# Kernel tuning notes

Hardware: AMD Instinct MI355X
Metric: run time of the kernel (lower is better)

Reference implementation:

```python
import jax, jax.numpy as jnp
import numpy as np

N = 50000        # nodes
E = 800000       # edges (avg degree 16)
IN_DIM = 256
H = 8            # heads
D = 32           # out_dim per head
T = 4            # edge_type_num
F = 16           # edge_feature_dim
NEG_SLOPE = 0.2


def setup_inputs() -> dict:
    key = jax.random.key(0)
    ks = jax.random.split(key, 9)
    feat = jax.random.normal(ks[0], (N, IN_DIM), dtype=jnp.float32)
    e_pro = jax.random.normal(ks[1], (E, F), dtype=jnp.float32)
    mask = jax.random.uniform(ks[2], (E, T), dtype=jnp.float32)
    W_n = jax.random.normal(ks[3], (IN_DIM, H * D), dtype=jnp.float32) * (1.0 / np.sqrt(IN_DIM))
    attn_l = jax.random.normal(ks[4], (H, D, T), dtype=jnp.float32) * 0.1
    attn_r = jax.random.normal(ks[5], (H, D, T), dtype=jnp.float32) * 0.1
    attn_m = jax.random.normal(ks[6], (H, F, T), dtype=jnp.float32) * 0.1
    src = jax.random.randint(ks[7], (E,), 0, N, dtype=jnp.int32)
    dst = jax.random.randint(ks[8], (E,), 0, N, dtype=jnp.int32)
    return {"feat": feat, "e_pro": e_pro, "mask": mask, "W_n": W_n,
            "attn_l": attn_l, "attn_r": attn_r, "attn_m": attn_m,
            "src": src, "dst": dst}


def reference(feat, e_pro, mask, W_n, attn_l, attn_r, attn_m, src, dst):
    # node projection: [N, H, D]
    feat_src = (feat @ W_n).reshape(N, H, D)

    # per-node attention logits per edge type: [N, H, T]
    el = jnp.einsum("nhd,hdt->nht", feat_src, attn_l)
    er = jnp.einsum("nhd,hdt->nht", feat_src, attn_r)
    # per-edge logits per edge type: [E, H, T]
    em = jnp.einsum("ef,hft->eht", e_pro, attn_m)

    # bmm with edge-type mask [E, T] -> scalar per head: [E, H]
    left = jnp.einsum("eht,et->eh", el[src], mask)
    right = jnp.einsum("eht,et->eh", er[dst], mask)
    em_e = jnp.einsum("eht,et->eh", em, mask)

    e = (left + right + em_e) / 3.0
    e = jnp.where(e > 0, e, NEG_SLOPE * e)  # leaky_relu

    # edge softmax over incoming edges of each dst node (stable)
    e_max = jax.ops.segment_max(e, dst, num_segments=N)          # [N, H]
    e_exp = jnp.exp(e - e_max[dst])                               # [E, H]
    e_sum = jax.ops.segment_sum(e_exp, dst, num_segments=N)      # [N, H]
    a = e_exp / e_sum[dst]                                       # [E, H]

    # u_mul_e + sum aggregation: [E, H, D] -> [N, H, D]
    msg = feat_src[src] * a[:, :, None]
    rst = jax.ops.segment_sum(msg, dst, num_segments=N)

    # cat=True: concat heads
    return rst.reshape(N, H * D)
```

## Files before the change

kernel.cpp:

```cpp
#include <hip/hip_runtime.h>
#include <hip/hip_bf16.h>
#include <hip/hip_fp16.h>

#define NN 50000
#define NEDGE 800000
#define INDIM 256
#define NH 8
#define ND 32
#define HD 256
#define NT 4
#define NF 16

typedef __attribute__((ext_vector_type(8))) short s16x8;
typedef __attribute__((ext_vector_type(4))) float f32x4;
typedef unsigned short u16;

__device__ __forceinline__ float bf2f(u16 u) {
    return __uint_as_float(((unsigned int)u) << 16);
}
__device__ __forceinline__ u16 f2bf(float f) {
    __hip_bfloat16 h = __float2bfloat16(f);
    return *reinterpret_cast<u16*>(&h);
}
__device__ __forceinline__ u16 f2h(float f) {
    __half h = __float2half(f);
    return *reinterpret_cast<u16*>(&h);
}
__device__ __forceinline__ float h2f(u16 u) {
    __half h = *reinterpret_cast<__half*>(&u);
    return __half2float(h);
}

__global__ __launch_bounds__(256) void prep_kernel(const float* __restrict__ W,
                                                   u16* __restrict__ Wt,
                                                   int* __restrict__ cnt,
                                                   int* __restrict__ cursor)
{
    int idx = blockIdx.x * 256 + threadIdx.x;
    int k = idx >> 8, c = idx & 255;
    Wt[(size_t)c * 256 + k] = f2bf(W[idx]);
    if (idx < NN) { cnt[idx] = 0; cursor[idx] = 0; }
}

__global__ __launch_bounds__(256) void gemm_mfma(
    const float* __restrict__ feat, const u16* __restrict__ Wt,
    const int* __restrict__ dst, int* __restrict__ cnt,
    u16* __restrict__ fs, int nrows)
{
    const int tid = threadIdx.x;
    {
        int e0 = (blockIdx.x * 256 + tid) * 2;
        if (e0 < NEDGE)     atomicAdd(&cnt[dst[e0]], 1);
        if (e0 + 1 < NEDGE) atomicAdd(&cnt[dst[e0 + 1]], 1);
    }

    __shared__ u16 At[32 * 256];
    const int brow = blockIdx.x * 32;

    #pragma unroll
    for (int it = 0; it < 4; ++it) {
        int fo = it * 2048 + tid * 8;
        int row = fo >> 8, col = fo & 255;
        int grow = brow + row;
        if (grow >= nrows) grow = nrows - 1;
        const float* gp = feat + (size_t)grow * 256 + col;
        float4 x = *reinterpret_cast<const float4*>(gp);
        float4 y = *reinterpret_cast<const float4*>(gp + 4);
        s16x8 v;
        v[0] = (short)f2bf(x.x); v[1] = (short)f2bf(x.y);
        v[2] = (short)f2bf(x.z); v[3] = (short)f2bf(x.w);
        v[4] = (short)f2bf(y.x); v[5] = (short)f2bf(y.y);
        v[6] = (short)f2bf(y.z); v[7] = (short)f2bf(y.w);
        int byte = (col * 2) ^ ((row & 7) << 4);
        *reinterpret_cast<s16x8*>((char*)At + row * 512 + byte) = v;
    }
    __syncthreads();

    const int wave = tid >> 6, lane = tid & 63;
    const int c0 = wave * 64;
    const int rA = lane & 15;
    const int kg = lane >> 4;

    f32x4 acc[2][4] = {};

    for (int k0 = 0; k0 < 256; k0 += 32) {
        const int kk = k0 + kg * 8;
        const int byte = (kk * 2) ^ ((rA & 7) << 4);
        s16x8 a0 = *reinterpret_cast<const s16x8*>((char*)At + rA * 512 + byte);
        s16x8 a1 = *reinterpret_cast<const s16x8*>((char*)At + (16 + rA) * 512 + byte);
        #pragma unroll
        for (int ct = 0; ct < 4; ++ct) {
            s16x8 b = *reinterpret_cast<const s16x8*>(Wt + (size_t)(c0 + ct * 16 + rA) * 256 + kk);
            acc[0][ct] = __builtin_amdgcn_mfma_f32_16x16x32_bf16(a0, b, acc[0][ct], 0, 0, 0);
            acc[1][ct] = __builtin_amdgcn_mfma_f32_16x16x32_bf16(a1, b, acc[1][ct], 0, 0, 0);
        }
    }

    #pragma unroll
    for (int rt = 0; rt < 2; ++rt) {
        #pragma unroll
        for (int r = 0; r < 4; ++r) {
            int row = brow + rt * 16 + kg * 4 + r;
            if (row < nrows) {
                #pragma unroll
                for (int ct = 0; ct < 4; ++ct) {
                    fs[(size_t)row * 256 + c0 + ct * 16 + rA] = f2bf(acc[rt][ct][r]);
                }
            }
        }
    }
}

__global__ __launch_bounds__(256) void elr_kernel(
    const u16* __restrict__ fs,
    const float* __restrict__ attn_l, const float* __restrict__ attn_r,
    u16* __restrict__ el, u16* __restrict__ er, int n)
{
    __shared__ float s_al[NH * ND * NT];
    __shared__ float s_ar[NH * ND * NT];
    for (int i = threadIdx.x; i < NH * ND * NT; i += 256) {
        s_al[i] = attn_l[i];
        s_ar[i] = attn_r[i];
    }
    __syncthreads();
    int wv = threadIdx.x >> 6, lane = threadIdx.x & 63;
    int node = blockIdx.x * 4 + wv;
    if (node >= n) return;
    int h = lane >> 3, j0 = (lane & 7) * 4;
    ushort4 u = *reinterpret_cast<const ushort4*>(fs + (size_t)node * HD + lane * 4);
    float f0 = bf2f(u.x), f1 = bf2f(u.y), f2 = bf2f(u.z), f3 = bf2f(u.w);
    const float* al = s_al + h * (ND * NT) + j0 * NT;
    const float* ar = s_ar + h * (ND * NT) + j0 * NT;
    float pl[NT], pr[NT];
    #pragma unroll
    for (int t = 0; t < NT; ++t) {
        pl[t] = f0*al[t] + f1*al[NT + t] + f2*al[2*NT + t] + f3*al[3*NT + t];
        pr[t] = f0*ar[t] + f1*ar[NT + t] + f2*ar[2*NT + t] + f3*ar[3*NT + t];
    }
    #pragma unroll
    for (int d = 1; d < 8; d <<= 1) {
        #pragma unroll
        for (int t = 0; t < NT; ++t) {
            pl[t] += __shfl_xor(pl[t], d);
            pr[t] += __shfl_xor(pr[t], d);
        }
    }
    if ((lane & 7) == 0) {
        ushort4 ol, orr;
        ol.x = f2h(pl[0]); ol.y = f2h(pl[1]); ol.z = f2h(pl[2]); ol.w = f2h(pl[3]);
        orr.x = f2h(pr[0]); orr.y = f2h(pr[1]); orr.z = f2h(pr[2]); orr.w = f2h(pr[3]);
        *reinterpret_cast<ushort4*>(el + (size_t)node * (NH*NT) + h * NT) = ol;
        *reinterpret_cast<ushort4*>(er + (size_t)node * (NH*NT) + h * NT) = orr;
    }
}

__global__ void scan1_kernel(const int* __restrict__ cnt, int* __restrict__ off,
                             int* __restrict__ blksum, int n) {
    __shared__ int sm[256];
    int i = blockIdx.x * 256 + threadIdx.x;
    int v = (i < n) ? cnt[i] : 0;
    sm[threadIdx.x] = v;
    __syncthreads();
    for (int d = 1; d < 256; d <<= 1) {
        int t = (threadIdx.x >= d) ? sm[threadIdx.x - d] : 0;
        __syncthreads();
        sm[threadIdx.x] += t;
        __syncthreads();
    }
    if (i < n) off[i] = sm[threadIdx.x] - v;
    if (threadIdx.x == 255) blksum[blockIdx.x] = sm[255];
}

__global__ void scan2_kernel(int* blksum, int nb) {
    __shared__ int sm[256];
    int v = (threadIdx.x < nb) ? blksum[threadIdx.x] : 0;
    sm[threadIdx.x] = v;
    __syncthreads();
    for (int d = 1; d < 256; d <<= 1) {
        int t = (threadIdx.x >= d) ? sm[threadIdx.x - d] : 0;
        __syncthreads();
        sm[threadIdx.x] += t;
        __syncthreads();
    }
    blksum[threadIdx.x] = sm[threadIdx.x] - v;
}

__global__ void scan3_kernel(int* __restrict__ off, const int* __restrict__ blksum,
                             int n, int ne) {
    int i = blockIdx.x * 256 + threadIdx.x;
    if (i < n) off[i] += blksum[blockIdx.x];
    if (i == 0) off[n] = ne;
}

__global__ __launch_bounds__(256) void edge_kernel(
    const float* __restrict__ e_pro, const float* __restrict__ mask,
    const float* __restrict__ attn_m,
    const int* __restrict__ src, const int* __restrict__ dst,
    const u16* __restrict__ el, const u16* __restrict__ er,
    const int* __restrict__ off, int* __restrict__ cursor,
    int* __restrict__ eIdx, u16* __restrict__ ev, int ne)
{
    __shared__ float4 s_am4[NF][NH];
    __shared__ float s_ep[32][17];
    __shared__ float s_mk[32][5];
    const int tid = threadIdx.x;
    const int eb = blockIdx.x * 32;

    for (int i = tid; i < NH * NF; i += 256) {
        int h = i >> 4, f = i & 15;
        const float* p = attn_m + (size_t)h * (NF * NT) + f * NT;
        s_am4[f][h] = make_float4(p[0], p[1], p[2], p[3]);
    }
    {
        int f2i = tid * 2;
        float2 v = *reinterpret_cast<const float2*>(e_pro + (size_t)eb * NF + f2i);
        int e_l = f2i >> 4, f = f2i & 15;
        s_ep[e_l][f] = v.x; s_ep[e_l][f + 1] = v.y;
    }
    if (tid < 128) {
        s_mk[tid >> 2][tid & 3] = mask[(size_t)eb * NT + tid];
    }
    __syncthreads();

    int e = eb + (tid >> 3);
    const int el_ = tid >> 3 & 31;
    const int j = tid & 7;

    int s = src[e], d = dst[e];
    float4 mk = make_float4(s_mk[el_][0], s_mk[el_][1], s_mk[el_][2], s_mk[el_][3]);

    union { uint2 v; u16 u[4]; } lv, rv;
    lv.v = *reinterpret_cast<const uint2*>(el + (size_t)s * (NH*NT) + j * NT);
    rv.v = *reinterpret_cast<const uint2*>(er + (size_t)d * (NH*NT) + j * NT);

    float em = 0.f;
    #pragma unroll
    for (int f = 0; f < NF; ++f) {
        float4 am = s_am4[f][j];
        float amm = mk.x*am.x + mk.y*am.y + mk.z*am.z + mk.w*am.w;
        em = fmaf(s_ep[el_][f], amm, em);
    }
    float left  = mk.x*h2f(lv.u[0]) + mk.y*h2f(lv.u[1]) + mk.z*h2f(lv.u[2]) + mk.w*h2f(lv.u[3]);
    float right = mk.x*h2f(rv.u[0]) + mk.y*h2f(rv.u[1]) + mk.z*h2f(rv.u[2]) + mk.w*h2f(rv.u[3]);

    float v = (left + right + em) * (1.0f / 3.0f);
    v = v > 0.f ? v : 0.2f * v;
    ev[(size_t)e * NH + j] = f2h(__expf(v));

    if (j == 0) {
        int p = atomicAdd(&cursor[d], 1);
        eIdx[off[d] + p] = e;
    }
}

__global__ __launch_bounds__(256) void agg_kernel(
    const int* __restrict__ off, const int* __restrict__ eIdx,
    const int* __restrict__ src, const u16* __restrict__ ev,
    const u16* __restrict__ fs, float* __restrict__ out, int n)
{
    int wv = threadIdx.x >> 6, lane = threadIdx.x & 63;
    int node = blockIdx.x * 4 + wv;
    if (node >= n) return;
    int beg = off[node], end = off[node + 1];
    int deg = end - beg;

    int h = lane & 7, sub = lane >> 3;
    float vc[8];
    int sc[8];
    float s = 0.f;
    #pragma unroll
    for (int slot = 0; slot < 8; ++slot) {
        int i = beg + slot * 8 + sub;
        float v = 0.f; int sn = 0;
        if (i < end) {
            int e = eIdx[i];
            v = h2f(ev[(size_t)e * NH + h]);
            sn = src[e];
        }
        vc[slot] = v; sc[slot] = sn; s += v;
    }
    for (int i = beg + 64 + sub; i < end; i += 8) {
        int e = eIdx[i];
        s += h2f(ev[(size_t)e * NH + h]);
    }
    s += __shfl_xor(s, 8);
    s += __shfl_xor(s, 16);
    s += __shfl_xor(s, 32);

    int h2 = lane >> 3;
    float S = __shfl(s, h2);
    float invS = S > 0.f ? 1.f / S : 0.f;
    const int col = lane * 4;
    float a0 = 0.f, a1 = 0.f, a2 = 0.f, a3 = 0.f;
    int nchunk = deg < 64 ? (deg + 7) >> 3 : 8;
    #pragma unroll
    for (int c = 0; c < 8; ++c) {
        if (c >= nchunk) break;
        float w8 = vc[c];
        int s8 = sc[c];
        #pragma unroll
        for (int q = 0; q < 8; ++q) {
            float w = __shfl(w8, q * 8 + h2);
            int sn  = __shfl(s8, q * 8 + h2);
            ushort4 u = *reinterpret_cast<const ushort4*>(fs + (size_t)sn * HD + col);
            a0 = fmaf(w, bf2f(u.x), a0); a1 = fmaf(w, bf2f(u.y), a1);
            a2 = fmaf(w, bf2f(u.z), a2); a3 = fmaf(w, bf2f(u.w), a3);
        }
    }
    for (int i = beg + 64; i < end; ++i) {
        int e = eIdx[i];
        float w = h2f(ev[(size_t)e * NH + h2]);
        int sn = src[e];
        ushort4 u = *reinterpret_cast<const ushort4*>(fs + (size_t)sn * HD + col);
        a0 = fmaf(w, bf2f(u.x), a0); a1 = fmaf(w, bf2f(u.y), a1);
        a2 = fmaf(w, bf2f(u.z), a2); a3 = fmaf(w, bf2f(u.w), a3);
    }
    a0 *= invS; a1 *= invS; a2 *= invS; a3 *= invS;
    *reinterpret_cast<float4*>(&out[(size_t)node * HD + col]) = make_float4(a0, a1, a2, a3);
}

extern "C" void kernel_launch(void* const* d_in, const int* in_sizes, int n_in,
                              void* d_out, int out_size, void* d_ws, size_t ws_size,
                              hipStream_t stream)
{
    const float* feat   = (const float*)d_in[0];
    const float* e_pro  = (const float*)d_in[1];
    const float* mask   = (const float*)d_in[2];
    const float* W_n    = (const float*)d_in[3];
    const float* attn_l = (const float*)d_in[4];
    const float* attn_r = (const float*)d_in[5];
    const float* attn_m = (const float*)d_in[6];
    const int* src      = (const int*)d_in[7];
    const int* dst      = (const int*)d_in[8];
    float* out = (float*)d_out;

    char* ws = (char*)d_ws;
    size_t o = 0;
    auto alloc = [&](size_t bytes) -> void* {
        void* p = (void*)(ws + o);
        o += (bytes + 255) & ~(size_t)255;
        return p;
    };
    u16* fs     = (u16*)alloc((size_t)NN * HD * 2);
    u16* Wt     = (u16*)alloc((size_t)INDIM * HD * 2);
    u16* el     = (u16*)alloc((size_t)NN * NH * NT * 2);
    u16* er     = (u16*)alloc((size_t)NN * NH * NT * 2);
    u16* ev     = (u16*)alloc((size_t)NEDGE * NH * 2);
    int* eIdx   = (int*)alloc((size_t)NEDGE * 4);
    int* cnt    = (int*)alloc((size_t)NN * 4);
    int* cursor = (int*)alloc((size_t)NN * 4);
    int* offs   = (int*)alloc((size_t)(NN + 1) * 4);
    int* blksum = (int*)alloc(256 * 4);
    (void)ws_size; (void)in_sizes; (void)n_in; (void)out_size;

    dim3 b256(256);
    hipLaunchKernelGGL(prep_kernel, dim3(256), b256, 0, stream, W_n, Wt, cnt, cursor);
    hipLaunchKernelGGL(gemm_mfma, dim3((NN + 31) / 32), b256, 0, stream, feat, Wt, dst, cnt, fs, NN);
    hipLaunchKernelGGL(elr_kernel, dim3((NN + 3) / 4), b256, 0, stream, fs, attn_l, attn_r, el, er, NN);
    hipLaunchKernelGGL(scan1_kernel, dim3((NN + 255) / 256), b256, 0, stream, cnt, offs, blksum, NN);
    hipLaunchKernelGGL(scan2_kernel, dim3(1), b256, 0, stream, blksum, (NN + 255) / 256);
    hipLaunchKernelGGL(scan3_kernel, dim3((NN + 255) / 256), b256, 0, stream, offs, blksum, NN, NEDGE);
    hipLaunchKernelGGL(edge_kernel, dim3(NEDGE / 32), b256, 0, stream,
                       e_pro, mask, attn_m, src, dst, el, er, offs, cursor, eIdx, ev, NEDGE);
    hipLaunchKernelGGL(agg_kernel, dim3((NN + 3) / 4), b256, 0, stream,
                       offs, eIdx, src, ev, fs, out, NN);
}
```

Measured before the change: 242.6 us.

## Store (edge, src) pairs in CSR, batch gathers, fuse softmax sum into aggregation

The edge kernel now writes (edge id, src) pairs into the CSR slot array, so the aggregation kernel no longer does a dependent src[e] lookup. The atomic slot reservation and the el/er gathers are issued before the shared-memory staging to overlap their latency. In the aggregation kernel, the separate softmax-denominator pass and its cross-lane reductions are dropped: each lane accumulates the weight sum alongside the weighted features, and the eight feature gathers per chunk are issued together before the FMAs for more memory-level parallelism. The cost is a larger index array (8 bytes per edge) and more registers held for the batched loads.

```diff
diff --git a/kernel.cpp b/kernel.cpp
--- a/kernel.cpp
+++ b/kernel.cpp
@@ -198,13 +198,24 @@
     const int* __restrict__ src, const int* __restrict__ dst,
     const u16* __restrict__ el, const u16* __restrict__ er,
     const int* __restrict__ off, int* __restrict__ cursor,
-    int* __restrict__ eIdx, u16* __restrict__ ev, int ne)
+    int2* __restrict__ es, u16* __restrict__ ev, int ne)
 {
     __shared__ float4 s_am4[NF][NH];
     __shared__ float s_ep[32][17];
     __shared__ float s_mk[32][5];
     const int tid = threadIdx.x;
     const int eb = blockIdx.x * 32;
+    const int j = tid & 7;
+    const int el_ = (tid >> 3) & 31;
+    const int e = eb + (tid >> 3);
+
+    int s = src[e], d = dst[e];
+    int slot = 0;
+    if (j == 0) slot = off[d] + atomicAdd(&cursor[d], 1);
+
+    union { uint2 v; u16 u[4]; } lv, rv;
+    lv.v = *reinterpret_cast<const uint2*>(el + (size_t)s * (NH*NT) + j * NT);
+    rv.v = *reinterpret_cast<const uint2*>(er + (size_t)d * (NH*NT) + j * NT);
 
     for (int i = tid; i < NH * NF; i += 256) {
         int h = i >> 4, f = i & 15;
@@ -222,16 +233,7 @@
     }
     __syncthreads();
 
-    int e = eb + (tid >> 3);
-    const int el_ = tid >> 3 & 31;
-    const int j = tid & 7;
-
-    int s = src[e], d = dst[e];
     float4 mk = make_float4(s_mk[el_][0], s_mk[el_][1], s_mk[el_][2], s_mk[el_][3]);
-
-    union { uint2 v; u16 u[4]; } lv, rv;
-    lv.v = *reinterpret_cast<const uint2*>(el + (size_t)s * (NH*NT) + j * NT);
-    rv.v = *reinterpret_cast<const uint2*>(er + (size_t)d * (NH*NT) + j * NT);
 
     float em = 0.f;
     #pragma unroll
@@ -247,16 +249,13 @@
     v = v > 0.f ? v : 0.2f * v;
     ev[(size_t)e * NH + j] = f2h(__expf(v));
 
-    if (j == 0) {
-        int p = atomicAdd(&cursor[d], 1);
-        eIdx[off[d] + p] = e;
-    }
+    if (j == 0) es[slot] = make_int2(e, s);
 }
 
 __global__ __launch_bounds__(256) void agg_kernel(
-    const int* __restrict__ off, const int* __restrict__ eIdx,
-    const int* __restrict__ src, const u16* __restrict__ ev,
-    const u16* __restrict__ fs, float* __restrict__ out, int n)
+    const int* __restrict__ off, const int2* __restrict__ es,
+    const u16* __restrict__ ev, const u16* __restrict__ fs,
+    float* __restrict__ out, int n)
 {
     int wv = threadIdx.x >> 6, lane = threadIdx.x & 63;
     int node = blockIdx.x * 4 + wv;
@@ -267,54 +266,56 @@
     int h = lane & 7, sub = lane >> 3;
     float vc[8];
     int sc[8];
-    float s = 0.f;
     #pragma unroll
     for (int slot = 0; slot < 8; ++slot) {
         int i = beg + slot * 8 + sub;
         float v = 0.f; int sn = 0;
         if (i < end) {
-            int e = eIdx[i];
-            v = h2f(ev[(size_t)e * NH + h]);
-            sn = src[e];
-        }
-        vc[slot] = v; sc[slot] = sn; s += v;
-    }
-    for (int i = beg + 64 + sub; i < end; i += 8) {
-        int e = eIdx[i];
-        s += h2f(ev[(size_t)e * NH + h]);
-    }
-    s += __shfl_xor(s, 8);
-    s += __shfl_xor(s, 16);
-    s += __shfl_xor(s, 32);
+            int2 p = es[i];
+            v = h2f(ev[(size_t)p.x * NH + h]);
+            sn = p.y;
+        }
+        vc[slot] = v; sc[slot] = sn;
+    }
 
     int h2 = lane >> 3;
-    float S = __shfl(s, h2);
-    float invS = S > 0.f ? 1.f / S : 0.f;
     const int col = lane * 4;
-    float a0 = 0.f, a1 = 0.f, a2 = 0.f, a3 = 0.f;
-    int nchunk = deg < 64 ? (deg + 7) >> 3 : 8;
+    float a0 = 0.f, a1 = 0.f, a2 = 0.f, a3 = 0.f, sw = 0.f;
+    int deg_ = deg < 64 ? deg : 64;
+    int nchunk = (deg_ + 7) >> 3;
     #pragma unroll
     for (int c = 0; c < 8; ++c) {
         if (c >= nchunk) break;
         float w8 = vc[c];
         int s8 = sc[c];
+        float w[8]; int sn[8];
         #pragma unroll
         for (int q = 0; q < 8; ++q) {
-            float w = __shfl(w8, q * 8 + h2);
-            int sn  = __shfl(s8, q * 8 + h2);
-            ushort4 u = *reinterpret_cast<const ushort4*>(fs + (size_t)sn * HD + col);
-            a0 = fmaf(w, bf2f(u.x), a0); a1 = fmaf(w, bf2f(u.y), a1);
-            a2 = fmaf(w, bf2f(u.z), a2); a3 = fmaf(w, bf2f(u.w), a3);
+            w[q]  = __shfl(w8, q * 8 + h2);
+            sn[q] = __shfl(s8, q * 8 + h2);
+        }
+        ushort4 u[8];
+        #pragma unroll
+        for (int q = 0; q < 8; ++q)
+            u[q] = *reinterpret_cast<const ushort4*>(fs + (size_t)sn[q] * HD + col);
+        #pragma unroll
+        for (int q = 0; q < 8; ++q) {
+            sw += w[q];
+            a0 = fmaf(w[q], bf2f(u[q].x), a0);
+            a1 = fmaf(w[q], bf2f(u[q].y), a1);
+            a2 = fmaf(w[q], bf2f(u[q].z), a2);
+            a3 = fmaf(w[q], bf2f(u[q].w), a3);
         }
     }
     for (int i = beg + 64; i < end; ++i) {
-        int e = eIdx[i];
-        float w = h2f(ev[(size_t)e * NH + h2]);
-        int sn = src[e];
-        ushort4 u = *reinterpret_cast<const ushort4*>(fs + (size_t)sn * HD + col);
+        int2 p = es[i];
+        float w = h2f(ev[(size_t)p.x * NH + h2]);
+        sw += w;
+        ushort4 u = *reinterpret_cast<const ushort4*>(fs + (size_t)p.y * HD + col);
         a0 = fmaf(w, bf2f(u.x), a0); a1 = fmaf(w, bf2f(u.y), a1);
         a2 = fmaf(w, bf2f(u.z), a2); a3 = fmaf(w, bf2f(u.w), a3);
     }
+    float invS = sw > 0.f ? 1.f / sw : 0.f;
     a0 *= invS; a1 *= invS; a2 *= invS; a3 *= invS;
     *reinterpret_cast<float4*>(&out[(size_t)node * HD + col]) = make_float4(a0, a1, a2, a3);
 }
@@ -346,7 +347,7 @@
     u16* el     = (u16*)alloc((size_t)NN * NH * NT * 2);
     u16* er     = (u16*)alloc((size_t)NN * NH * NT * 2);
     u16* ev     = (u16*)alloc((size_t)NEDGE * NH * 2);
-    int* eIdx   = (int*)alloc((size_t)NEDGE * 4);
+    int2* es    = (int2*)alloc((size_t)NEDGE * 8);
     int* cnt    = (int*)alloc((size_t)NN * 4);
     int* cursor = (int*)alloc((size_t)NN * 4);
     int* offs   = (int*)alloc((size_t)(NN + 1) * 4);
@@ -361,7 +362,7 @@
     hipLaunchKernelGGL(scan2_kernel, dim3(1), b256, 0, stream, blksum, (NN + 255) / 256);
     hipLaunchKernelGGL(scan3_kernel, dim3((NN + 255) / 256), b256, 0, stream, offs, blksum, NN, NEDGE);
     hipLaunchKernelGGL(edge_kernel, dim3(NEDGE / 32), b256, 0, stream,
-                       e_pro, mask, attn_m, src, dst, el, er, offs, cursor, eIdx, ev, NEDGE);
+                       e_pro, mask, attn_m, src, dst, el, er, offs, cursor, es, ev, NEDGE);
     hipLaunchKernelGGL(agg_kernel, dim3((NN + 3) / 4), b256, 0, stream,
-                       offs, eIdx, src, ev, fs, out, NN);
-}
+                       offs, es, ev, fs, out, NN);
+}
```

Measured after the change: 232.0 us. 1.05x faster.
